# Kernel tuning notes

Measured on AMD Instinct MI355X. Metric: run time of the kernel, lower is better.

## Reference

```python
import jax, jax.numpy as jnp
import numpy as np

N_SRC, N_DST, E = 50000, 50000, 800000
D_GT, D_AG = 64, 64
HID, HEADS = 256, 4
FPH = HID // HEADS  # 64
N_ACT = 16
NEG_SLOPE = 0.2  # DGL GATv2Conv default negative_slope


def setup_inputs() -> dict:
    key = jax.random.key(0)
    ks = jax.random.split(key, 16)
    f32 = jnp.float32
    return {
        "feat_gt": jax.random.normal(ks[0], (N_SRC, D_GT), f32),
        "feat_agent": jax.random.normal(ks[1], (N_DST, D_AG), f32),
        "h0": jax.random.normal(ks[2], (N_DST, HID), f32),
        "edge_src": jax.random.randint(ks[3], (E,), 0, N_SRC),
        "edge_dst": jax.random.randint(ks[4], (E,), 0, N_DST),
        "W_src": jax.random.normal(ks[5], (D_GT, HID), f32) * 0.1,
        "b_src": jnp.zeros((HID,), f32),
        "W_dst": jax.random.normal(ks[6], (D_AG, HID), f32) * 0.1,
        "b_dst": jnp.zeros((HID,), f32),
        "attn": jax.random.normal(ks[7], (HEADS, FPH), f32) * 0.1,
        "W_res": jax.random.normal(ks[8], (D_AG, HID), f32) * 0.1,
        "b_res": jnp.zeros((HID,), f32),
        "W_ih": jax.random.normal(ks[9], (3 * HID, HID), f32) * 0.05,
        "W_hh": jax.random.normal(ks[10], (3 * HID, HID), f32) * 0.05,
        "b_ih": jnp.zeros((3 * HID,), f32),
        "b_hh": jnp.zeros((3 * HID,), f32),
        "W_out": jax.random.normal(ks[11], (HID, N_ACT), f32) * 0.05,
        "b_out": jnp.zeros((N_ACT,), f32),
    }


def _gatv2(feat_gt, feat_agent, edge_src, edge_dst,
           W_src, b_src, W_dst, b_dst, attn, W_res, b_res):
    # GATv2Conv (bipartite, share_weights=False, residual=True, activation=ReLU)
    fs = (feat_gt @ W_src + b_src).reshape(N_SRC, HEADS, FPH)    # [Ns,H,F]
    fd = (feat_agent @ W_dst + b_dst).reshape(N_DST, HEADS, FPH)  # [Nd,H,F]
    e = fs[edge_src] + fd[edge_dst]                               # [E,H,F]
    e = jnp.where(e > 0, e, NEG_SLOPE * e)                        # LeakyReLU
    score = jnp.einsum('ehf,hf->eh', e, attn)                     # [E,H]
    # edge softmax segmented by destination node
    smax = jax.lax.stop_gradient(
        jax.ops.segment_max(score, edge_dst, num_segments=N_DST))  # [Nd,H]
    ex = jnp.exp(score - smax[edge_dst])
    den = jax.ops.segment_sum(ex, edge_dst, num_segments=N_DST)   # [Nd,H]
    alpha = ex / den[edge_dst]                                    # [E,H]
    msg = alpha[:, :, None] * fs[edge_src]                        # [E,H,F]
    rst = jax.ops.segment_sum(msg, edge_dst, num_segments=N_DST)  # [Nd,H,F]
    rst = rst.reshape(N_DST, HID) + (feat_agent @ W_res + b_res)  # residual
    return jax.nn.relu(rst)


def _gru_cell(x, h, W_ih, W_hh, b_ih, b_hh):
    gi = x @ W_ih.T + b_ih
    gh = h @ W_hh.T + b_hh
    ir, iz, inn = jnp.split(gi, 3, axis=-1)
    hr, hz, hn = jnp.split(gh, 3, axis=-1)
    r = jax.nn.sigmoid(ir + hr)
    z = jax.nn.sigmoid(iz + hz)
    n = jnp.tanh(inn + r * hn)
    return (1.0 - z) * n + z * h


def reference(feat_gt, feat_agent, h0, edge_src, edge_dst,
              W_src, b_src, W_dst, b_dst, attn, W_res, b_res,
              W_ih, W_hh, b_ih, b_hh, W_out, b_out):
    x = _gatv2(feat_gt, feat_agent, edge_src, edge_dst,
               W_src, b_src, W_dst, b_dst, attn, W_res, b_res)  # [Nd,HID]
    h = _gru_cell(x, h0, W_ih, W_hh, b_ih, b_hh)                # [Nd,HID]
    logits = h @ W_out + b_out                                  # [Nd,N_ACT]
    return (logits, h)
```

## Files before the change

kernel.cpp:

```cpp
#include <hip/hip_runtime.h>
#include <stdint.h>

#define N_SRCN 50000
#define N_DSTN 50000
#define NE     800000
#define HIDN   256
#define NEG    0.2f

typedef __attribute__((ext_vector_type(8)))  short short8;
typedef __attribute__((ext_vector_type(16))) float float16v;

__device__ __forceinline__ float bf2f(unsigned short u){
    union { unsigned u32; float f; } c; c.u32 = ((unsigned)u) << 16; return c.f;
}
__device__ __forceinline__ unsigned short f2bf(float f){
    union { float f; unsigned u; } c; c.f = f;
    unsigned r = c.u + 0x7fffu + ((c.u >> 16) & 1u);
    return (unsigned short)(r >> 16);
}
__device__ __forceinline__ float4 ld4b(const unsigned short* p){
    uint2 u = *reinterpret_cast<const uint2*>(p);
    float4 r;
    r.x = bf2f((unsigned short)(u.x & 0xffff));
    r.y = bf2f((unsigned short)(u.x >> 16));
    r.z = bf2f((unsigned short)(u.y & 0xffff));
    r.w = bf2f((unsigned short)(u.y >> 16));
    return r;
}

__global__ void pack_kernel(const float* __restrict__ Wsrc, const float* __restrict__ Wdst,
                            const float* __restrict__ Wres, const float* __restrict__ Wih,
                            const float* __restrict__ Whh,
                            unsigned short* __restrict__ Wt2,
                            unsigned short* __restrict__ Wf){
    int i = blockIdx.x * 256 + threadIdx.x;
    if (i < 49152){
        int which = i >> 14, j = i & 16383;
        int k = j >> 8, c = j & 255;
        const float* W = (which == 0) ? Wsrc : (which == 1 ? Wdst : Wres);
        float v = W[j];
        int off = which * 16384 + (c >> 5) * 2048 + (k >> 4) * 512
                + (((k >> 3) & 1) * 32 + (c & 31)) * 8 + (k & 7);
        Wt2[off] = f2bf(v);
    } else if (i < 49152 + 196608){
        int o = i - 49152;
        int row = o >> 8, k = o & 255;
        int g = row >> 8, c = row & 255;
        float v = Wih[o];
        int off = g * 131072 + (c >> 5) * 16384 + (k >> 4) * 512
                + (((k >> 3) & 1) * 32 + (c & 31)) * 8 + (k & 7);
        Wf[off] = f2bf(v);
    } else if (i < 49152 + 393216){
        int o = i - 49152 - 196608;
        int row = o >> 8, k = o & 255;
        int g = row >> 8, c = row & 255;
        float v = Whh[o];
        int off = g * 131072 + (c >> 5) * 16384 + (16 + (k >> 4)) * 512
                + (((k >> 3) & 1) * 32 + (c & 31)) * 8 + (k & 7);
        Wf[off] = f2bf(v);
    }
}

__global__ __launch_bounds__(256) void proj_kernel(
        const float* __restrict__ Agt, const float* __restrict__ Aag,
        const unsigned short* __restrict__ Wt2,
        const float* __restrict__ bsrc, const float* __restrict__ bdst,
        const float* __restrict__ bres,
        unsigned short* __restrict__ fs, unsigned short* __restrict__ fd,
        unsigned short* __restrict__ resb){
    __shared__ unsigned short As[64 * 72];
    __shared__ unsigned short Cs[64 * 72];
    int z = blockIdx.z;
    const float* A = (z == 0) ? Agt : Aag;
    const float* bias = (z == 0) ? bsrc : (z == 1 ? bdst : bres);
    unsigned short* out = (z == 0) ? fs : (z == 1 ? fd : resb);
    const unsigned short* Wb = Wt2 + z * 16384;
    int tid = threadIdx.x;
    int m0 = blockIdx.y * 64;
    #pragma unroll
    for (int i = 0; i < 4; ++i){
        int ci = tid + i * 256;
        int row = ci >> 4;
        int k4 = (ci & 15) << 2;
        int gr = m0 + row; if (gr >= N_SRCN) gr = N_SRCN - 1;
        float4 v = *reinterpret_cast<const float4*>(A + (size_t)gr * 64 + k4);
        unsigned short* dp = As + row * 72 + k4;
        dp[0] = f2bf(v.x); dp[1] = f2bf(v.y); dp[2] = f2bf(v.z); dp[3] = f2bf(v.w);
    }
    __syncthreads();
    int lane = tid & 63, w = tid >> 6;
    int l31 = lane & 31, half = lane >> 5;
    int msub = (w & 1) * 32;
    int cbw = blockIdx.x * 2 + (w >> 1);
    const unsigned short* bb = Wb + cbw * 2048 + lane * 8;
    const unsigned short* ap = As + (msub + l31) * 72 + half * 8;
    float16v acc = {0,0,0,0,0,0,0,0,0,0,0,0,0,0,0,0};
    #pragma unroll
    for (int ks = 0; ks < 4; ++ks){
        short8 a = *reinterpret_cast<const short8*>(ap + ks * 16);
        short8 b = *reinterpret_cast<const short8*>(bb + ks * 512);
        acc = __builtin_amdgcn_mfma_f32_32x32x16_bf16(a, b, acc, 0, 0, 0);
    }
    float bv = bias[cbw * 32 + l31];
    int ccol = (w >> 1) * 32 + l31;
    #pragma unroll
    for (int r = 0; r < 16; ++r){
        int row = (r & 3) + 8 * (r >> 2) + 4 * half + msub;
        Cs[row * 72 + ccol] = f2bf(acc[r] + bv);
    }
    __syncthreads();
    int srow = tid >> 2, chunk = tid & 3;
    int gr2 = m0 + srow;
    if (gr2 < N_SRCN){
        const uint4* sp = reinterpret_cast<const uint4*>(Cs + srow * 72 + chunk * 16);
        uint4* gp = reinterpret_cast<uint4*>(out + (size_t)gr2 * 256 + blockIdx.x * 64 + chunk * 16);
        gp[0] = sp[0];
        gp[1] = sp[1];
    }
}

__global__ void degree_kernel(const int* __restrict__ dst, int* __restrict__ deg){
    int i = blockIdx.x * 256 + threadIdx.x;
    if (i < NE) atomicAdd(&deg[dst[i]], 1);
}

__global__ void scan1_kernel(const int* __restrict__ deg, int* __restrict__ bsum){
    __shared__ int s[256];
    int tid = threadIdx.x;
    int i = blockIdx.x * 256 + tid;
    s[tid] = (i < N_DSTN) ? deg[i] : 0;
    __syncthreads();
    #pragma unroll
    for (int off = 128; off; off >>= 1){
        if (tid < off) s[tid] += s[tid + off];
        __syncthreads();
    }
    if (tid == 0) bsum[blockIdx.x] = s[0];
}

__global__ void scan2_kernel(const int* __restrict__ bsum, int* __restrict__ boff){
    __shared__ int s[256];
    int tid = threadIdx.x;
    int v = (tid < 196) ? bsum[tid] : 0;
    s[tid] = v;
    __syncthreads();
    #pragma unroll
    for (int off = 1; off < 256; off <<= 1){
        int t = (tid >= off) ? s[tid - off] : 0;
        __syncthreads();
        s[tid] += t;
        __syncthreads();
    }
    if (tid < 196) boff[tid] = s[tid] - v;
}

__global__ void scan3_kernel(const int* __restrict__ deg, const int* __restrict__ boff,
                             int* __restrict__ ptr, int* __restrict__ cursor){
    __shared__ int s[256];
    int tid = threadIdx.x;
    int i = blockIdx.x * 256 + tid;
    int v = (i < N_DSTN) ? deg[i] : 0;
    s[tid] = v;
    __syncthreads();
    #pragma unroll
    for (int off = 1; off < 256; off <<= 1){
        int t = (tid >= off) ? s[tid - off] : 0;
        __syncthreads();
        s[tid] += t;
        __syncthreads();
    }
    int ex = s[tid] - v + boff[blockIdx.x];
    if (i < N_DSTN){ ptr[i] = ex; cursor[i] = ex; }
}

__global__ void scatter_kernel(const int* __restrict__ src, const int* __restrict__ dst,
                               int* __restrict__ cursor, int* __restrict__ csr){
    int i = blockIdx.x * 256 + threadIdx.x;
    if (i < NE){
        int d = dst[i];
        int pos = atomicAdd(&cursor[d], 1);
        csr[pos] = src[i];
    }
}

__global__ __launch_bounds__(256) void aggregate_kernel(
        const unsigned short* __restrict__ fs, const unsigned short* __restrict__ fd,
        const unsigned short* __restrict__ res, const float* __restrict__ attn,
        const int* __restrict__ ptr, const int* __restrict__ deg,
        const int* __restrict__ csr, unsigned short* __restrict__ x){
    int wv = threadIdx.x >> 6;
    int d = blockIdx.x * 4 + wv;
    if (d >= N_DSTN) return;
    int lane = threadIdx.x & 63;
    int c4 = lane * 4;
    float4 fdv = ld4b(fd + (size_t)d * 256 + c4);
    float4 at = *reinterpret_cast<const float4*>(attn + (lane >> 4) * 64 + (lane & 15) * 4);
    int p = ptr[d], dg = deg[d];
    float l = 0.f;
    float4 acc = make_float4(0.f, 0.f, 0.f, 0.f);
    for (int base = 0; base < dg; base += 64){
        int cnt = min(64, dg - base);
        int sreg = (lane < cnt) ? csr[p + base + lane] : 0;
        float4 b0 = ld4b(fs + (size_t)__shfl(sreg, 0) * 256 + c4);
        float4 b1 = ld4b(fs + (size_t)__shfl(sreg, 1 & 63) * 256 + c4);
        float4 b2 = ld4b(fs + (size_t)__shfl(sreg, 2 & 63) * 256 + c4);
        float4 b3 = ld4b(fs + (size_t)__shfl(sreg, 3 & 63) * 256 + c4);
        for (int j = 0; j < cnt; j += 4){
            float4 n0 = ld4b(fs + (size_t)__shfl(sreg, (j + 4) & 63) * 256 + c4);
            float4 n1 = ld4b(fs + (size_t)__shfl(sreg, (j + 5) & 63) * 256 + c4);
            float4 n2 = ld4b(fs + (size_t)__shfl(sreg, (j + 6) & 63) * 256 + c4);
            float4 n3 = ld4b(fs + (size_t)__shfl(sreg, (j + 7) & 63) * 256 + c4);
#define PROC(BV, T) { \
            float ex = BV.x + fdv.x; ex = ex > 0.f ? ex : NEG * ex; \
            float ey = BV.y + fdv.y; ey = ey > 0.f ? ey : NEG * ey; \
            float ez = BV.z + fdv.z; ez = ez > 0.f ? ez : NEG * ez; \
            float ew = BV.w + fdv.w; ew = ew > 0.f ? ew : NEG * ew; \
            float part = ex * at.x + ey * at.y + ez * at.z + ew * at.w; \
            part += __shfl_xor(part, 1); \
            part += __shfl_xor(part, 2); \
            part += __shfl_xor(part, 4); \
            part += __shfl_xor(part, 8); \
            float wgt = ((j + (T)) < cnt) ? __expf(part) : 0.f; \
            l += wgt; \
            acc.x = fmaf(wgt, BV.x, acc.x); \
            acc.y = fmaf(wgt, BV.y, acc.y); \
            acc.z = fmaf(wgt, BV.z, acc.z); \
            acc.w = fmaf(wgt, BV.w, acc.w); }
            PROC(b0, 0) PROC(b1, 1) PROC(b2, 2) PROC(b3, 3)
#undef PROC
            b0 = n0; b1 = n1; b2 = n2; b3 = n3;
        }
    }
    float inv = (l > 0.f) ? 1.f / l : 0.f;
    float4 rv = ld4b(res + (size_t)d * 256 + c4);
    float xx = fmaxf(fmaf(acc.x, inv, rv.x), 0.f);
    float xy = fmaxf(fmaf(acc.y, inv, rv.y), 0.f);
    float xz = fmaxf(fmaf(acc.z, inv, rv.z), 0.f);
    float xw = fmaxf(fmaf(acc.w, inv, rv.w), 0.f);
    uint2 o;
    o.x = (unsigned)f2bf(xx) | ((unsigned)f2bf(xy) << 16);
    o.y = (unsigned)f2bf(xz) | ((unsigned)f2bf(xw) << 16);
    *reinterpret_cast<uint2*>(x + (size_t)d * 256 + c4) = o;
}

__global__ __launch_bounds__(256, 4) void gru_kernel(
        const unsigned short* __restrict__ Xb,
        const float* __restrict__ H0, const unsigned short* __restrict__ Wf,
        const float* __restrict__ bih, const float* __restrict__ bhh,
        float* __restrict__ outH){
    __shared__ unsigned short As[128 * 136];
    int tid = threadIdx.x;
    int sid = blockIdx.x;
    int xcd = sid & 7, rr_ = sid >> 3;
    int strip = xcd * 49 + (rr_ >> 3);
    int cb = rr_ & 7;
    int m0 = strip << 7;
    int w = tid >> 6, lane = tid & 63;
    int l31 = lane & 31, half = lane >> 5;
    int cg = cb * 32 + l31;
    const unsigned short* bb = Wf + cb * 16384 + lane * 8;
    float16v ar  = {0,0,0,0,0,0,0,0,0,0,0,0,0,0,0,0};
    float16v az = ar, anx = ar, anh = ar;
    #pragma unroll
    for (int kc = 0; kc < 512; kc += 128){
        __syncthreads();
        if (kc < 256){
            #pragma unroll
            for (int i = 0; i < 8; ++i){
                int ci = tid + i * 256;
                int row = ci >> 4;
                int k8 = (ci & 15) << 3;
                int gr = m0 + row; if (gr >= N_DSTN) gr = N_DSTN - 1;
                *reinterpret_cast<uint4*>(As + row * 136 + k8) =
                    *reinterpret_cast<const uint4*>(Xb + (size_t)gr * 256 + kc + k8);
            }
        } else {
            #pragma unroll
            for (int i = 0; i < 8; ++i){
                int ci = tid + i * 256;
                int row = ci >> 4;
                int k8 = (ci & 15) << 3;
                int gr = m0 + row; if (gr >= N_DSTN) gr = N_DSTN - 1;
                const float* hp = H0 + (size_t)gr * 256 + (kc - 256) + k8;
                float4 f0 = *reinterpret_cast<const float4*>(hp);
                float4 f1 = *reinterpret_cast<const float4*>(hp + 4);
                uint4 o;
                o.x = (unsigned)f2bf(f0.x) | ((unsigned)f2bf(f0.y) << 16);
                o.y = (unsigned)f2bf(f0.z) | ((unsigned)f2bf(f0.w) << 16);
                o.z = (unsigned)f2bf(f1.x) | ((unsigned)f2bf(f1.y) << 16);
                o.w = (unsigned)f2bf(f1.z) | ((unsigned)f2bf(f1.w) << 16);
                *reinterpret_cast<uint4*>(As + row * 136 + k8) = o;
            }
        }
        __syncthreads();
        const unsigned short* ap = As + (w * 32 + l31) * 136 + half * 8;
        #pragma unroll
        for (int ks = 0; ks < 8; ++ks){
            int kk = (kc >> 4) + ks;
            short8 a  = *reinterpret_cast<const short8*>(ap + ks * 16);
            short8 br = *reinterpret_cast<const short8*>(bb + (size_t)kk * 512);
            short8 bz = *reinterpret_cast<const short8*>(bb + 131072 + (size_t)kk * 512);
            short8 bn = *reinterpret_cast<const short8*>(bb + 262144 + (size_t)kk * 512);
            ar = __builtin_amdgcn_mfma_f32_32x32x16_bf16(a, br, ar, 0, 0, 0);
            az = __builtin_amdgcn_mfma_f32_32x32x16_bf16(a, bz, az, 0, 0, 0);
            if (kc < 256) anx = __builtin_amdgcn_mfma_f32_32x32x16_bf16(a, bn, anx, 0, 0, 0);
            else          anh = __builtin_amdgcn_mfma_f32_32x32x16_bf16(a, bn, anh, 0, 0, 0);
        }
    }
    float rb = bih[cg] + bhh[cg];
    float zb = bih[256 + cg] + bhh[256 + cg];
    float bin = bih[512 + cg], bhn = bhh[512 + cg];
    #pragma unroll
    for (int r = 0; r < 16; ++r){
        int m = m0 + w * 32 + (r & 3) + 8 * (r >> 2) + 4 * half;
        if (m < N_DSTN){
            float h0v = H0[(size_t)m * 256 + cg];
            float rrg = 1.f / (1.f + __expf(-(ar[r] + rb)));
            float zz = 1.f / (1.f + __expf(-(az[r] + zb)));
            float nx = anx[r] + bin + rrg * (anh[r] + bhn);
            float tm = __expf(-2.f * fabsf(nx));
            float nn = (1.f - tm) / (1.f + tm);
            nn = (nx >= 0.f) ? nn : -nn;
            outH[(size_t)m * 256 + cg] = (1.f - zz) * nn + zz * h0v;
        }
    }
}

__global__ __launch_bounds__(256) void logits_kernel(
        const float* __restrict__ H, const float* __restrict__ Wout,
        const float* __restrict__ bout, float* __restrict__ outL){
    __shared__ float Hl[16 * 260];
    __shared__ float Wl[16 * 260];
    int tid = threadIdx.x;
    int m0 = blockIdx.x * 16;
    #pragma unroll
    for (int i = 0; i < 4; ++i){
        int ci = tid + i * 256;
        int row = ci >> 6;
        int c4 = (ci & 63) << 2;
        int gr = m0 + row; if (gr >= N_DSTN) gr = N_DSTN - 1;
        float4 v = *reinterpret_cast<const float4*>(H + (size_t)gr * 256 + c4);
        float* dp = Hl + row * 260 + c4;
        dp[0] = v.x; dp[1] = v.y; dp[2] = v.z; dp[3] = v.w;
    }
    #pragma unroll
    for (int i = 0; i < 16; ++i){
        int ci = tid + i * 256;
        int c = ci >> 4, j = ci & 15;
        Wl[j * 260 + c] = Wout[c * 16 + j];
    }
    __syncthreads();
    int row = tid >> 4, j = tid & 15;
    const float* hr = Hl + row * 260;
    const float* wr = Wl + j * 260;
    float acc = bout[j];
    #pragma unroll
    for (int c = 0; c < 256; c += 4){
        float4 hv = *reinterpret_cast<const float4*>(hr + c);
        float4 wv = *reinterpret_cast<const float4*>(wr + c);
        acc = fmaf(hv.x, wv.x, fmaf(hv.y, wv.y, fmaf(hv.z, wv.z, fmaf(hv.w, wv.w, acc))));
    }
    int m = m0 + row;
    if (m < N_DSTN) outL[m * 16 + j] = acc;
}

extern "C" void kernel_launch(void* const* d_in, const int* in_sizes, int n_in,
                              void* d_out, int out_size, void* d_ws, size_t ws_size,
                              hipStream_t stream){
    const float* feat_gt = (const float*)d_in[0];
    const float* feat_ag = (const float*)d_in[1];
    const float* h0      = (const float*)d_in[2];
    const int*   e_src   = (const int*)d_in[3];
    const int*   e_dst   = (const int*)d_in[4];
    const float* W_src   = (const float*)d_in[5];
    const float* b_src   = (const float*)d_in[6];
    const float* W_dst   = (const float*)d_in[7];
    const float* b_dst   = (const float*)d_in[8];
    const float* attn    = (const float*)d_in[9];
    const float* W_res   = (const float*)d_in[10];
    const float* b_res   = (const float*)d_in[11];
    const float* W_ih    = (const float*)d_in[12];
    const float* W_hh    = (const float*)d_in[13];
    const float* b_ih    = (const float*)d_in[14];
    const float* b_hh    = (const float*)d_in[15];
    const float* W_out   = (const float*)d_in[16];
    const float* b_out   = (const float*)d_in[17];

    float* outL = (float*)d_out;
    float* outH = outL + (size_t)N_DSTN * 16;

    char* ws = (char*)d_ws;
    size_t off = 0;
    auto alloc = [&](size_t bytes) -> void* {
        void* p = ws + off; off = (off + bytes + 255) & ~(size_t)255; return p;
    };
    unsigned short* fs   = (unsigned short*)alloc((size_t)N_SRCN * 256 * 2);
    unsigned short* fd   = (unsigned short*)alloc((size_t)N_DSTN * 256 * 2);
    unsigned short* res  = (unsigned short*)alloc((size_t)N_DSTN * 256 * 2);
    unsigned short* xb   = (unsigned short*)alloc((size_t)N_DSTN * 256 * 2);
    unsigned short* Wt2  = (unsigned short*)alloc(49152 * 2);
    unsigned short* Wf   = (unsigned short*)alloc(393216 * 2);
    int* deg    = (int*)alloc(N_DSTN * 4);
    int* ptr    = (int*)alloc(N_DSTN * 4);
    int* cursor = (int*)alloc(N_DSTN * 4);
    int* csr    = (int*)alloc((size_t)NE * 4);
    int* bsum   = (int*)alloc(256 * 4);
    int* boff   = (int*)alloc(256 * 4);

    hipMemsetAsync(deg, 0, N_DSTN * 4, stream);
    pack_kernel<<<1728, 256, 0, stream>>>(W_src, W_dst, W_res, W_ih, W_hh, Wt2, Wf);

    proj_kernel<<<dim3(4, 782, 3), 256, 0, stream>>>(feat_gt, feat_ag, Wt2,
                                                     b_src, b_dst, b_res, fs, fd, res);

    degree_kernel<<<3125, 256, 0, stream>>>(e_dst, deg);
    scan1_kernel<<<196, 256, 0, stream>>>(deg, bsum);
    scan2_kernel<<<1, 256, 0, stream>>>(bsum, boff);
    scan3_kernel<<<196, 256, 0, stream>>>(deg, boff, ptr, cursor);
    scatter_kernel<<<3125, 256, 0, stream>>>(e_src, e_dst, cursor, csr);
    aggregate_kernel<<<12500, 256, 0, stream>>>(fs, fd, res, attn, ptr, deg, csr, xb);

    gru_kernel<<<3136, 256, 0, stream>>>(xb, h0, Wf, b_ih, b_hh, outH);
    logits_kernel<<<3125, 256, 0, stream>>>(outH, W_out, b_out, outL);
}
```

Baseline: 485.1 us.

## Restructure GRU GEMM to full-width 64-row tiles with swizzled LDS

The GRU kernel now assigns each 512-thread block a 64-row strip covering all 256 output columns. The whole 64x512 bf16 A tile (x concatenated with bf16-converted h0) is loaded into LDS once, using an XOR swizzle to avoid bank conflicts. Previously, 128-row tiles were reloaded for each of 8 column blocks, which meant the X and H0 rows were read and converted eight times. Each wave now computes two 32-column tiles for all three gates, which doubles accumulator registers and lowers blocks per CU.

```diff
diff --git a/kernel.cpp b/kernel.cpp
--- a/kernel.cpp
+++ b/kernel.cpp
@@ -243,87 +243,107 @@
     *reinterpret_cast<uint2*>(x + (size_t)d * 256 + c4) = o;
 }
 
-__global__ __launch_bounds__(256, 4) void gru_kernel(
+__global__ __launch_bounds__(512, 2) void gru_kernel(
         const unsigned short* __restrict__ Xb,
         const float* __restrict__ H0, const unsigned short* __restrict__ Wf,
         const float* __restrict__ bih, const float* __restrict__ bhh,
         float* __restrict__ outH){
-    __shared__ unsigned short As[128 * 136];
-    int tid = threadIdx.x;
-    int sid = blockIdx.x;
-    int xcd = sid & 7, rr_ = sid >> 3;
-    int strip = xcd * 49 + (rr_ >> 3);
-    int cb = rr_ & 7;
-    int m0 = strip << 7;
+    __shared__ unsigned short As[64 * 512];
+    int tid = threadIdx.x;
+    int m0 = blockIdx.x << 6;
+    #pragma unroll
+    for (int i = 0; i < 4; ++i){
+        int ci = tid + i * 512;
+        int row = ci >> 5, c = ci & 31;
+        int gr = m0 + row; if (gr >= N_DSTN) gr = N_DSTN - 1;
+        *reinterpret_cast<uint4*>(As + row * 512 + ((c ^ (row & 7)) << 3)) =
+            *reinterpret_cast<const uint4*>(Xb + (size_t)gr * 256 + (c << 3));
+    }
+    #pragma unroll
+    for (int i = 0; i < 4; ++i){
+        int ci = tid + i * 512;
+        int row = ci >> 5, c = ci & 31;
+        int gr = m0 + row; if (gr >= N_DSTN) gr = N_DSTN - 1;
+        const float* hp = H0 + (size_t)gr * 256 + (c << 3);
+        float4 f0 = *reinterpret_cast<const float4*>(hp);
+        float4 f1 = *reinterpret_cast<const float4*>(hp + 4);
+        uint4 o;
+        o.x = (unsigned)f2bf(f0.x) | ((unsigned)f2bf(f0.y) << 16);
+        o.y = (unsigned)f2bf(f0.z) | ((unsigned)f2bf(f0.w) << 16);
+        o.z = (unsigned)f2bf(f1.x) | ((unsigned)f2bf(f1.y) << 16);
+        o.w = (unsigned)f2bf(f1.z) | ((unsigned)f2bf(f1.w) << 16);
+        *reinterpret_cast<uint4*>(As + row * 512 + (((c + 32) ^ (row & 7)) << 3)) = o;
+    }
+    __syncthreads();
     int w = tid >> 6, lane = tid & 63;
     int l31 = lane & 31, half = lane >> 5;
-    int cg = cb * 32 + l31;
-    const unsigned short* bb = Wf + cb * 16384 + lane * 8;
-    float16v ar  = {0,0,0,0,0,0,0,0,0,0,0,0,0,0,0,0};
-    float16v az = ar, anx = ar, anh = ar;
-    #pragma unroll
-    for (int kc = 0; kc < 512; kc += 128){
-        __syncthreads();
-        if (kc < 256){
-            #pragma unroll
-            for (int i = 0; i < 8; ++i){
-                int ci = tid + i * 256;
-                int row = ci >> 4;
-                int k8 = (ci & 15) << 3;
-                int gr = m0 + row; if (gr >= N_DSTN) gr = N_DSTN - 1;
-                *reinterpret_cast<uint4*>(As + row * 136 + k8) =
-                    *reinterpret_cast<const uint4*>(Xb + (size_t)gr * 256 + kc + k8);
-            }
-        } else {
-            #pragma unroll
-            for (int i = 0; i < 8; ++i){
-                int ci = tid + i * 256;
-                int row = ci >> 4;
-                int k8 = (ci & 15) << 3;
-                int gr = m0 + row; if (gr >= N_DSTN) gr = N_DSTN - 1;
-                const float* hp = H0 + (size_t)gr * 256 + (kc - 256) + k8;
-                float4 f0 = *reinterpret_cast<const float4*>(hp);
-                float4 f1 = *reinterpret_cast<const float4*>(hp + 4);
-                uint4 o;
-                o.x = (unsigned)f2bf(f0.x) | ((unsigned)f2bf(f0.y) << 16);
-                o.y = (unsigned)f2bf(f0.z) | ((unsigned)f2bf(f0.w) << 16);
-                o.z = (unsigned)f2bf(f1.x) | ((unsigned)f2bf(f1.y) << 16);
-                o.w = (unsigned)f2bf(f1.z) | ((unsigned)f2bf(f1.w) << 16);
-                *reinterpret_cast<uint4*>(As + row * 136 + k8) = o;
-            }
-        }
-        __syncthreads();
-        const unsigned short* ap = As + (w * 32 + l31) * 136 + half * 8;
-        #pragma unroll
-        for (int ks = 0; ks < 8; ++ks){
-            int kk = (kc >> 4) + ks;
-            short8 a  = *reinterpret_cast<const short8*>(ap + ks * 16);
-            short8 br = *reinterpret_cast<const short8*>(bb + (size_t)kk * 512);
-            short8 bz = *reinterpret_cast<const short8*>(bb + 131072 + (size_t)kk * 512);
-            short8 bn = *reinterpret_cast<const short8*>(bb + 262144 + (size_t)kk * 512);
-            ar = __builtin_amdgcn_mfma_f32_32x32x16_bf16(a, br, ar, 0, 0, 0);
-            az = __builtin_amdgcn_mfma_f32_32x32x16_bf16(a, bz, az, 0, 0, 0);
-            if (kc < 256) anx = __builtin_amdgcn_mfma_f32_32x32x16_bf16(a, bn, anx, 0, 0, 0);
-            else          anh = __builtin_amdgcn_mfma_f32_32x32x16_bf16(a, bn, anh, 0, 0, 0);
-        }
-    }
-    float rb = bih[cg] + bhh[cg];
-    float zb = bih[256 + cg] + bhh[256 + cg];
-    float bin = bih[512 + cg], bhn = bhh[512 + cg];
-    #pragma unroll
-    for (int r = 0; r < 16; ++r){
-        int m = m0 + w * 32 + (r & 3) + 8 * (r >> 2) + 4 * half;
-        if (m < N_DSTN){
-            float h0v = H0[(size_t)m * 256 + cg];
-            float rrg = 1.f / (1.f + __expf(-(ar[r] + rb)));
-            float zz = 1.f / (1.f + __expf(-(az[r] + zb)));
-            float nx = anx[r] + bin + rrg * (anh[r] + bhn);
-            float tm = __expf(-2.f * fabsf(nx));
-            float nn = (1.f - tm) / (1.f + tm);
-            nn = (nx >= 0.f) ? nn : -nn;
-            outH[(size_t)m * 256 + cg] = (1.f - zz) * nn + zz * h0v;
-        }
-    }
+    int rt = w >> 2, cp = w & 3;
+    int arow = rt * 32 + l31;
+    int rl = arow & 7;
+    const unsigned short* apb = As + arow * 512;
+    const unsigned short* b0r = Wf + (size_t)(2 * cp) * 16384 + lane * 8;
+    const unsigned short* b0z = b0r + 131072;
+    const unsigned short* b0n = b0r + 262144;
+    const unsigned short* b1r = b0r + 16384;
+    const unsigned short* b1z = b1r + 131072;
+    const unsigned short* b1n = b1r + 262144;
+    float16v zv = {0,0,0,0,0,0,0,0,0,0,0,0,0,0,0,0};
+    float16v ar0 = zv, az0 = zv, an0 = zv, ah0 = zv;
+    float16v ar1 = zv, az1 = zv, an1 = zv, ah1 = zv;
+    #pragma unroll
+    for (int kk = 0; kk < 16; ++kk){
+        short8 a = *reinterpret_cast<const short8*>(apb + (((kk * 2 + half) ^ rl) << 3));
+        short8 vr0 = *reinterpret_cast<const short8*>(b0r + kk * 512);
+        short8 vz0 = *reinterpret_cast<const short8*>(b0z + kk * 512);
+        short8 vn0 = *reinterpret_cast<const short8*>(b0n + kk * 512);
+        short8 vr1 = *reinterpret_cast<const short8*>(b1r + kk * 512);
+        short8 vz1 = *reinterpret_cast<const short8*>(b1z + kk * 512);
+        short8 vn1 = *reinterpret_cast<const short8*>(b1n + kk * 512);
+        ar0 = __builtin_amdgcn_mfma_f32_32x32x16_bf16(a, vr0, ar0, 0, 0, 0);
+        az0 = __builtin_amdgcn_mfma_f32_32x32x16_bf16(a, vz0, az0, 0, 0, 0);
+        an0 = __builtin_amdgcn_mfma_f32_32x32x16_bf16(a, vn0, an0, 0, 0, 0);
+        ar1 = __builtin_amdgcn_mfma_f32_32x32x16_bf16(a, vr1, ar1, 0, 0, 0);
+        az1 = __builtin_amdgcn_mfma_f32_32x32x16_bf16(a, vz1, az1, 0, 0, 0);
+        an1 = __builtin_amdgcn_mfma_f32_32x32x16_bf16(a, vn1, an1, 0, 0, 0);
+    }
+    #pragma unroll
+    for (int kk = 16; kk < 32; ++kk){
+        short8 a = *reinterpret_cast<const short8*>(apb + (((kk * 2 + half) ^ rl) << 3));
+        short8 vr0 = *reinterpret_cast<const short8*>(b0r + kk * 512);
+        short8 vz0 = *reinterpret_cast<const short8*>(b0z + kk * 512);
+        short8 vn0 = *reinterpret_cast<const short8*>(b0n + kk * 512);
+        short8 vr1 = *reinterpret_cast<const short8*>(b1r + kk * 512);
+        short8 vz1 = *reinterpret_cast<const short8*>(b1z + kk * 512);
+        short8 vn1 = *reinterpret_cast<const short8*>(b1n + kk * 512);
+        ar0 = __builtin_amdgcn_mfma_f32_32x32x16_bf16(a, vr0, ar0, 0, 0, 0);
+        az0 = __builtin_amdgcn_mfma_f32_32x32x16_bf16(a, vz0, az0, 0, 0, 0);
+        ah0 = __builtin_amdgcn_mfma_f32_32x32x16_bf16(a, vn0, ah0, 0, 0, 0);
+        ar1 = __builtin_amdgcn_mfma_f32_32x32x16_bf16(a, vr1, ar1, 0, 0, 0);
+        az1 = __builtin_amdgcn_mfma_f32_32x32x16_bf16(a, vz1, az1, 0, 0, 0);
+        ah1 = __builtin_amdgcn_mfma_f32_32x32x16_bf16(a, vn1, ah1, 0, 0, 0);
+    }
+#define EPI(AR, AZ, AN, AH, CT) { \
+    int cg = (cp * 2 + (CT)) * 32 + l31; \
+    float rb = bih[cg] + bhh[cg]; \
+    float zb = bih[256 + cg] + bhh[256 + cg]; \
+    float bin = bih[512 + cg], bhn = bhh[512 + cg]; \
+    _Pragma("unroll") \
+    for (int r = 0; r < 16; ++r){ \
+        int m = m0 + rt * 32 + (r & 3) + 8 * (r >> 2) + 4 * half; \
+        if (m < N_DSTN){ \
+            float h0v = H0[(size_t)m * 256 + cg]; \
+            float rrg = 1.f / (1.f + __expf(-((AR)[r] + rb))); \
+            float zg  = 1.f / (1.f + __expf(-((AZ)[r] + zb))); \
+            float nx = (AN)[r] + bin + rrg * ((AH)[r] + bhn); \
+            float tm = __expf(-2.f * fabsf(nx)); \
+            float nn = (1.f - tm) / (1.f + tm); \
+            nn = (nx >= 0.f) ? nn : -nn; \
+            outH[(size_t)m * 256 + cg] = (1.f - zg) * nn + zg * h0v; \
+        } \
+    } }
+    EPI(ar0, az0, an0, ah0, 0)
+    EPI(ar1, az1, an1, ah1, 1)
+#undef EPI
 }
 
 __global__ __launch_bounds__(256) void logits_kernel(
@@ -420,6 +440,6 @@
     scatter_kernel<<<3125, 256, 0, stream>>>(e_src, e_dst, cursor, csr);
     aggregate_kernel<<<12500, 256, 0, stream>>>(fs, fd, res, attn, ptr, deg, csr, xb);
 
-    gru_kernel<<<3136, 256, 0, stream>>>(xb, h0, Wf, b_ih, b_hh, outH);
+    gru_kernel<<<782, 512, 0, stream>>>(xb, h0, Wf, b_ih, b_hh, outH);
     logits_kernel<<<3125, 256, 0, stream>>>(outH, W_out, b_out, outL);
 }
```

After: 605.3 us. 24.8% more time.

## Restructure GRU GEMM to load each row tile once for all column blocks

Applied to the files above, without the earlier changes.

The GRU kernel now uses 1024-thread blocks that each own 64 rows and all 256 output columns. The full K=512 activation tile (X plus H0 converted to bf16) is staged into shared memory once, using an XOR swizzle to avoid bank conflicts. Previously each 128-row strip was reloaded and re-converted by 8 separate column-block workgroups in four K chunks with extra barriers. The cost is 64KB of LDS per block and large blocks, which may reduce occupancy and leaves no overlap between loading and MFMA.

```diff
diff --git a/kernel.cpp b/kernel.cpp
--- a/kernel.cpp
+++ b/kernel.cpp
@@ -243,85 +243,85 @@
     *reinterpret_cast<uint2*>(x + (size_t)d * 256 + c4) = o;
 }
 
-__global__ __launch_bounds__(256, 4) void gru_kernel(
+__global__ __launch_bounds__(1024, 4) void gru_kernel(
         const unsigned short* __restrict__ Xb,
         const float* __restrict__ H0, const unsigned short* __restrict__ Wf,
         const float* __restrict__ bih, const float* __restrict__ bhh,
         float* __restrict__ outH){
-    __shared__ unsigned short As[128 * 136];
-    int tid = threadIdx.x;
-    int sid = blockIdx.x;
-    int xcd = sid & 7, rr_ = sid >> 3;
-    int strip = xcd * 49 + (rr_ >> 3);
-    int cb = rr_ & 7;
-    int m0 = strip << 7;
+    __shared__ unsigned short As[64 * 512];
+    int tid = threadIdx.x;
+    int m0 = blockIdx.x << 6;
+    #pragma unroll
+    for (int i = 0; i < 2; ++i){
+        int ci = tid + i * 1024;
+        int row = ci >> 5, c = ci & 31;
+        int gr = m0 + row; if (gr >= N_DSTN) gr = N_DSTN - 1;
+        *reinterpret_cast<uint4*>(As + row * 512 + ((c ^ (row & 7)) << 3)) =
+            *reinterpret_cast<const uint4*>(Xb + (size_t)gr * 256 + (c << 3));
+    }
+    #pragma unroll
+    for (int i = 0; i < 2; ++i){
+        int ci = tid + i * 1024;
+        int row = ci >> 5, c = ci & 31;
+        int gr = m0 + row; if (gr >= N_DSTN) gr = N_DSTN - 1;
+        const float* hp = H0 + (size_t)gr * 256 + (c << 3);
+        float4 f0 = *reinterpret_cast<const float4*>(hp);
+        float4 f1 = *reinterpret_cast<const float4*>(hp + 4);
+        uint4 o;
+        o.x = (unsigned)f2bf(f0.x) | ((unsigned)f2bf(f0.y) << 16);
+        o.y = (unsigned)f2bf(f0.z) | ((unsigned)f2bf(f0.w) << 16);
+        o.z = (unsigned)f2bf(f1.x) | ((unsigned)f2bf(f1.y) << 16);
+        o.w = (unsigned)f2bf(f1.z) | ((unsigned)f2bf(f1.w) << 16);
+        *reinterpret_cast<uint4*>(As + row * 512 + (((c + 32) ^ (row & 7)) << 3)) = o;
+    }
+    __syncthreads();
     int w = tid >> 6, lane = tid & 63;
     int l31 = lane & 31, half = lane >> 5;
-    int cg = cb * 32 + l31;
-    const unsigned short* bb = Wf + cb * 16384 + lane * 8;
-    float16v ar  = {0,0,0,0,0,0,0,0,0,0,0,0,0,0,0,0};
-    float16v az = ar, anx = ar, anh = ar;
-    #pragma unroll
-    for (int kc = 0; kc < 512; kc += 128){
-        __syncthreads();
-        if (kc < 256){
-            #pragma unroll
-            for (int i = 0; i < 8; ++i){
-                int ci = tid + i * 256;
-                int row = ci >> 4;
-                int k8 = (ci & 15) << 3;
-                int gr = m0 + row; if (gr >= N_DSTN) gr = N_DSTN - 1;
-                *reinterpret_cast<uint4*>(As + row * 136 + k8) =
-                    *reinterpret_cast<const uint4*>(Xb + (size_t)gr * 256 + kc + k8);
-            }
-        } else {
-            #pragma unroll
-            for (int i = 0; i < 8; ++i){
-                int ci = tid + i * 256;
-                int row = ci >> 4;
-                int k8 = (ci & 15) << 3;
-                int gr = m0 + row; if (gr >= N_DSTN) gr = N_DSTN - 1;
-                const float* hp = H0 + (size_t)gr * 256 + (kc - 256) + k8;
-                float4 f0 = *reinterpret_cast<const float4*>(hp);
-                float4 f1 = *reinterpret_cast<const float4*>(hp + 4);
-                uint4 o;
-                o.x = (unsigned)f2bf(f0.x) | ((unsigned)f2bf(f0.y) << 16);
-                o.y = (unsigned)f2bf(f0.z) | ((unsigned)f2bf(f0.w) << 16);
-                o.z = (unsigned)f2bf(f1.x) | ((unsigned)f2bf(f1.y) << 16);
-                o.w = (unsigned)f2bf(f1.z) | ((unsigned)f2bf(f1.w) << 16);
-                *reinterpret_cast<uint4*>(As + row * 136 + k8) = o;
-            }
-        }
-        __syncthreads();
-        const unsigned short* ap = As + (w * 32 + l31) * 136 + half * 8;
-        #pragma unroll
-        for (int ks = 0; ks < 8; ++ks){
-            int kk = (kc >> 4) + ks;
-            short8 a  = *reinterpret_cast<const short8*>(ap + ks * 16);
-            short8 br = *reinterpret_cast<const short8*>(bb + (size_t)kk * 512);
-            short8 bz = *reinterpret_cast<const short8*>(bb + 131072 + (size_t)kk * 512);
-            short8 bn = *reinterpret_cast<const short8*>(bb + 262144 + (size_t)kk * 512);
-            ar = __builtin_amdgcn_mfma_f32_32x32x16_bf16(a, br, ar, 0, 0, 0);
-            az = __builtin_amdgcn_mfma_f32_32x32x16_bf16(a, bz, az, 0, 0, 0);
-            if (kc < 256) anx = __builtin_amdgcn_mfma_f32_32x32x16_bf16(a, bn, anx, 0, 0, 0);
-            else          anh = __builtin_amdgcn_mfma_f32_32x32x16_bf16(a, bn, anh, 0, 0, 0);
-        }
-    }
+    int rt = w >> 3, ct = w & 7;
+    int arow = rt * 32 + l31;
+    int rl = arow & 7;
+    const unsigned short* apb = As + arow * 512;
+    const unsigned short* br = Wf + (size_t)ct * 16384 + lane * 8;
+    const unsigned short* bz = br + 131072;
+    const unsigned short* bn = br + 262144;
+    float16v zv = {0,0,0,0,0,0,0,0,0,0,0,0,0,0,0,0};
+    float16v ar = zv, az = zv, anx = zv, anh = zv;
+    #pragma unroll
+    for (int kk = 0; kk < 16; ++kk){
+        short8 a  = *reinterpret_cast<const short8*>(apb + (((kk * 2 + half) ^ rl) << 3));
+        short8 vr = *reinterpret_cast<const short8*>(br + kk * 512);
+        short8 vz = *reinterpret_cast<const short8*>(bz + kk * 512);
+        short8 vn = *reinterpret_cast<const short8*>(bn + kk * 512);
+        ar  = __builtin_amdgcn_mfma_f32_32x32x16_bf16(a, vr, ar,  0, 0, 0);
+        az  = __builtin_amdgcn_mfma_f32_32x32x16_bf16(a, vz, az,  0, 0, 0);
+        anx = __builtin_amdgcn_mfma_f32_32x32x16_bf16(a, vn, anx, 0, 0, 0);
+    }
+    #pragma unroll
+    for (int kk = 16; kk < 32; ++kk){
+        short8 a  = *reinterpret_cast<const short8*>(apb + (((kk * 2 + half) ^ rl) << 3));
+        short8 vr = *reinterpret_cast<const short8*>(br + kk * 512);
+        short8 vz = *reinterpret_cast<const short8*>(bz + kk * 512);
+        short8 vn = *reinterpret_cast<const short8*>(bn + kk * 512);
+        ar  = __builtin_amdgcn_mfma_f32_32x32x16_bf16(a, vr, ar,  0, 0, 0);
+        az  = __builtin_amdgcn_mfma_f32_32x32x16_bf16(a, vz, az,  0, 0, 0);
+        anh = __builtin_amdgcn_mfma_f32_32x32x16_bf16(a, vn, anh, 0, 0, 0);
+    }
+    int cg = ct * 32 + l31;
     float rb = bih[cg] + bhh[cg];
     float zb = bih[256 + cg] + bhh[256 + cg];
     float bin = bih[512 + cg], bhn = bhh[512 + cg];
     #pragma unroll
     for (int r = 0; r < 16; ++r){
-        int m = m0 + w * 32 + (r & 3) + 8 * (r >> 2) + 4 * half;
+        int m = m0 + rt * 32 + (r & 3) + 8 * (r >> 2) + 4 * half;
         if (m < N_DSTN){
             float h0v = H0[(size_t)m * 256 + cg];
             float rrg = 1.f / (1.f + __expf(-(ar[r] + rb)));
-            float zz = 1.f / (1.f + __expf(-(az[r] + zb)));
+            float zg  = 1.f / (1.f + __expf(-(az[r] + zb)));
             float nx = anx[r] + bin + rrg * (anh[r] + bhn);
             float tm = __expf(-2.f * fabsf(nx));
             float nn = (1.f - tm) / (1.f + tm);
             nn = (nx >= 0.f) ? nn : -nn;
-            outH[(size_t)m * 256 + cg] = (1.f - zz) * nn + zz * h0v;
+            outH[(size_t)m * 256 + cg] = (1.f - zg) * nn + zg * h0v;
         }
     }
 }
@@ -420,6 +420,6 @@
     scatter_kernel<<<3125, 256, 0, stream>>>(e_src, e_dst, cursor, csr);
     aggregate_kernel<<<12500, 256, 0, stream>>>(fs, fd, res, attn, ptr, deg, csr, xb);
 
-    gru_kernel<<<3136, 256, 0, stream>>>(xb, h0, Wf, b_ih, b_hh, outH);
+    gru_kernel<<<782, 1024, 0, stream>>>(xb, h0, Wf, b_ih, b_hh, outH);
     logits_kernel<<<3125, 256, 0, stream>>>(outH, W_out, b_out, outL);
 }
```

Measured after the change: 486.8 us. About the same (+0.4%).
